# Kernel optimization log

Measured on AMD Instinct MI355X. Metric: run time of the kernel, lower is better.

The kernel has to match this reference:

```python
import jax, jax.numpy as jnp
import numpy as np

N_NODES = 50000
N_EDGES = 800000
HIDDEN = 128
HEADS = 8
HEAD_DIM = HIDDEN // HEADS
N_REL = 64
SCALE = np.sqrt(HEAD_DIM).astype(np.float32)


def setup_inputs() -> dict:
    key = jax.random.key(0)
    ks = jax.random.split(key, 12)
    s = 1.0 / np.sqrt(2 * HIDDEN)
    s2 = 1.0 / np.sqrt(HIDDEN)
    return {
        "node_features": jax.random.normal(ks[0], (N_NODES, HIDDEN), jnp.float32),
        "query_embedding": jax.random.normal(ks[1], (1, HIDDEN), jnp.float32),
        "relation_embeddings": jax.random.normal(ks[2], (N_REL, HIDDEN), jnp.float32),
        "Wq": jax.random.uniform(ks[3], (2 * HIDDEN, HIDDEN), jnp.float32, -s, s),
        "bq": jnp.zeros((HIDDEN,), jnp.float32),
        "Wk": jax.random.uniform(ks[4], (2 * HIDDEN, HIDDEN), jnp.float32, -s, s),
        "bk": jnp.zeros((HIDDEN,), jnp.float32),
        "Wv": jax.random.uniform(ks[5], (HIDDEN, HIDDEN), jnp.float32, -s2, s2),
        "bv": jnp.zeros((HIDDEN,), jnp.float32),
        "Wo": jax.random.uniform(ks[6], (HIDDEN, HIDDEN), jnp.float32, -s2, s2),
        "bo": jnp.zeros((HIDDEN,), jnp.float32),
        "edge_index": jax.random.randint(ks[7], (2, N_EDGES), 0, N_NODES, jnp.int64),
        "edge_type": jax.random.randint(ks[8], (N_EDGES,), 0, N_REL, jnp.int64),
    }


def reference(node_features, query_embedding, relation_embeddings,
              Wq, bq, Wk, bk, Wv, bv, Wo, bo, edge_index, edge_type):
    n = node_features.shape[0]
    # expand query to all nodes and concat: [N, 2*hidden]
    q_exp = jnp.broadcast_to(query_embedding, (n, HIDDEN))
    nq = jnp.concatenate([node_features, q_exp], axis=-1)
    q = (nq @ Wq + bq).reshape(n, HEADS, HEAD_DIM)
    k = (nq @ Wk + bk).reshape(n, HEADS, HEAD_DIM)
    v = (node_features @ Wv + bv).reshape(n, HEADS, HEAD_DIM)

    src, dst = edge_index[0], edge_index[1]
    rel_bias = relation_embeddings[edge_type].reshape(-1, HEADS, HEAD_DIM)

    # edge-wise scores [E, heads]
    scores = jnp.sum(q[dst] * (k[src] + rel_bias), axis=-1) / SCALE

    # sparse softmax grouped by dst; torch init of max buffer is 0 -> clamp at 0
    seg_max = jax.ops.segment_max(scores, dst, num_segments=n)
    seg_max = jnp.maximum(seg_max, 0.0)
    exp_s = jnp.exp(scores - seg_max[dst])
    seg_sum = jax.ops.segment_sum(exp_s, dst, num_segments=n)
    attn = exp_s / (seg_sum[dst] + 1e-8)  # [E, heads]

    messages = attn[:, :, None] * v[src]  # [E, heads, head_dim]
    out = jax.ops.segment_sum(messages, dst, num_segments=n)  # [N, heads, head_dim]
    out = out.reshape(n, HIDDEN)
    return out @ Wo + bo
```

## Files before the change

kernel.cpp:

```cpp
#include <hip/hip_runtime.h>
#include <math.h>

#define N_NODES 50000
#define N_EDGES 800000
#define HID 128
#define HEADS 8
#define HDIM 16
#define CAP 96
#define CNT_BLOCKS 3125
#define QKV_BLOCKS 782

typedef __attribute__((ext_vector_type(8))) short short8;
typedef __attribute__((ext_vector_type(4))) float floatx4;

#if defined(__has_builtin)
#if __has_builtin(__builtin_amdgcn_fdot2_f32_bf16)
#define HAVE_DOT2 1
#endif
#endif
#ifndef HAVE_DOT2
#define HAVE_DOT2 0
#endif

#if HAVE_DOT2
typedef __attribute__((ext_vector_type(2))) __bf16 bf16x2;
__device__ __forceinline__ float dot2acc(unsigned int a, unsigned int b, float c) {
    return __builtin_amdgcn_fdot2_f32_bf16(__builtin_bit_cast(bf16x2, a),
                                           __builtin_bit_cast(bf16x2, b), c, false);
}
#endif

__device__ __forceinline__ float bf_lo(unsigned int d) { return __uint_as_float(d << 16); }
__device__ __forceinline__ float bf_hi(unsigned int d) { return __uint_as_float(d & 0xFFFF0000u); }
__device__ __forceinline__ unsigned short f2bf(float f) {
    unsigned int u = __float_as_uint(f);
    u = (u + 0x7FFFu + ((u >> 16) & 1u)) >> 16;
    return (unsigned short)u;
}
__device__ __forceinline__ unsigned int pack_bf2(float a, float b) {
    return (unsigned int)f2bf(a) | ((unsigned int)f2bf(b) << 16);
}

__global__ __launch_bounds__(256) void prep_kernel(
    const float* __restrict__ query, const float* __restrict__ rel,
    const float* __restrict__ Wq, const float* __restrict__ bq,
    const float* __restrict__ Wk, const float* __restrict__ bk,
    const float* __restrict__ Wv, const float* __restrict__ Wo,
    unsigned short* __restrict__ Wt, unsigned short* __restrict__ relbf,
    int* __restrict__ counts, float* __restrict__ bqe, float* __restrict__ bke) {
    __shared__ float fred[256];
    int b = blockIdx.x, tid = threadIdx.x;
    if (b >= 256) {
        const float* W  = (b == 256) ? Wq : Wk;
        const float* bb = (b == 256) ? bq : bk;
        float* dst      = (b == 256) ? bqe : bke;
        int j = tid & 127;
        int half = tid >> 7;
        float a = 0.0f;
        int i0 = half * 64;
        for (int i = 0; i < 64; ++i) a += query[i0 + i] * W[(HID + i0 + i) * HID + j];
        fred[tid] = a;
        __syncthreads();
        if (half == 0) dst[j] = fred[j] + fred[128 + j] + bb[j];
        return;
    }
    int idx = b * 256 + tid;
    if (idx < N_NODES) counts[idx] = 0;
    if (idx < 64 * HID) relbf[idx] = f2bf(rel[idx]);
    int m = idx >> 14;
    int rem = idx & 16383;
    int n = rem >> 7, k = rem & 127;
    const float* W = (m == 0) ? Wq : (m == 1) ? Wk : (m == 2) ? Wv : Wo;
    Wt[idx] = f2bf(W[k * HID + n]);
}

__global__ __launch_bounds__(256) void qkv_bucket_kernel(
    const float* __restrict__ nf, const unsigned short* __restrict__ Wt,
    const float* __restrict__ bqe, const float* __restrict__ bke, const float* __restrict__ bv,
    const int* __restrict__ ei, const int* __restrict__ et,
    int* __restrict__ counts, unsigned int* __restrict__ slots,
    unsigned short* __restrict__ qb16, unsigned short* __restrict__ kv16) {
    if (blockIdx.x >= QKV_BLOCKS) {
        int e = (blockIdx.x - QKV_BLOCKS) * 256 + threadIdx.x;
        if (e < N_EDGES) {
            int dst = ei[N_EDGES + e];
            int pos = atomicAdd(&counts[dst], 1);
            if (pos < CAP)
                slots[(unsigned)dst * CAP + pos] =
                    ((unsigned int)et[e] << 18) | (unsigned int)ei[e];
        }
        return;
    }
    int row0 = blockIdx.x * 64;
    int wave = threadIdx.x >> 6;
    int lane = threadIdx.x & 63;
    int col  = lane & 15;
    int quad = lane >> 4;

    short8 afr[4][4];
    #pragma unroll
    for (int t = 0; t < 4; ++t) {
        int arow = row0 + t * 16 + col;
        int asafe = (arow < N_NODES) ? arow : (N_NODES - 1);
        #pragma unroll
        for (int kk = 0; kk < 4; ++kk) {
            const float4* ap = (const float4*)(nf + (size_t)asafe * HID + kk * 32 + quad * 8);
            float4 a0 = ap[0], a1 = ap[1];
            short8 f;
            f[0] = (short)f2bf(a0.x); f[1] = (short)f2bf(a0.y);
            f[2] = (short)f2bf(a0.z); f[3] = (short)f2bf(a0.w);
            f[4] = (short)f2bf(a1.x); f[5] = (short)f2bf(a1.y);
            f[6] = (short)f2bf(a1.z); f[7] = (short)f2bf(a1.w);
            afr[t][kk] = f;
        }
    }
    const float* biases[3] = {bqe, bke, bv};
    #pragma unroll
    for (int m = 0; m < 3; ++m) {
        const unsigned short* W = Wt + (size_t)m * HID * HID;
        #pragma unroll
        for (int nn = 0; nn < 2; ++nn) {
            int n = wave * 2 + nn;
            float b = biases[m][n * 16 + col];
            floatx4 acc[4];
            #pragma unroll
            for (int t = 0; t < 4; ++t) acc[t] = (floatx4){b, b, b, b};
            short8 bfr[4];
            #pragma unroll
            for (int kk = 0; kk < 4; ++kk)
                bfr[kk] = *(const short8*)(W + (size_t)(n * 16 + col) * HID + kk * 32 + quad * 8);
            #pragma unroll
            for (int kk = 0; kk < 4; ++kk)
                #pragma unroll
                for (int t = 0; t < 4; ++t)
                    acc[t] = __builtin_amdgcn_mfma_f32_16x16x32_bf16(afr[t][kk], bfr[kk], acc[t], 0, 0, 0);
            #pragma unroll
            for (int t = 0; t < 4; ++t) {
                #pragma unroll
                for (int i = 0; i < 4; ++i) {
                    int r = row0 + t * 16 + quad * 4 + i;
                    if (r < N_NODES) {
                        int c = n * 16 + col;
                        if (m == 0)      qb16[(size_t)r * HID + c] = f2bf(acc[t][i]);
                        else if (m == 1) kv16[(size_t)r * 256 + c] = f2bf(acc[t][i]);
                        else             kv16[(size_t)r * 256 + 128 + c] = f2bf(acc[t][i]);
                    }
                }
            }
        }
    }
}

__global__ __launch_bounds__(256) void attn_kernel(
    const unsigned int* __restrict__ qb, const unsigned int* __restrict__ kvu,
    const unsigned int* __restrict__ relu,
    const int* __restrict__ counts, const unsigned int* __restrict__ slots,
    unsigned int* __restrict__ abuf) {
    int node = blockIdx.x * 4 + (threadIdx.x >> 6);
    int lane = threadIdx.x & 63;
    int h = lane & 7;
    int hd = lane >> 3;
    int deg = counts[node];
    if (deg > CAP) deg = CAP;
    unsigned int rs = (unsigned)node * CAP;

    const uint4* qp = (const uint4*)(qb + (unsigned)node * 64 + h * 8);
    uint4 qa = qp[0], qc = qp[1];
#if !HAVE_DOT2
    float qf0 = bf_lo(qa.x), qf1 = bf_hi(qa.x), qf2 = bf_lo(qa.y), qf3 = bf_hi(qa.y);
    float qf4 = bf_lo(qa.z), qf5 = bf_hi(qa.z), qf6 = bf_lo(qa.w), qf7 = bf_hi(qa.w);
    float qf8 = bf_lo(qc.x), qf9 = bf_hi(qc.x), qf10 = bf_lo(qc.y), qf11 = bf_hi(qc.y);
    float qf12 = bf_lo(qc.z), qf13 = bf_hi(qc.z), qf14 = bf_lo(qc.w), qf15 = bf_hi(qc.w);
#endif

    int myel = hd;
    unsigned int pk = (myel < deg) ? slots[rs + myel] : 0u;
    float ssum = 0.0f, accx = 0.0f, accy = 0.0f;
    for (int base = 0; base < deg; base += 8) {
        int el = base + myel;
        int eln = el + 8;
        unsigned int pk_next = (eln < deg) ? slots[rs + eln] : 0u;
        unsigned int pw = 0u;
        if (el < deg) {
            unsigned int src = pk & 0x3FFFF;
            unsigned int etv = pk >> 18;
            const uint4* kp = (const uint4*)(kvu + (src << 7) + h * 8);
            uint4 ka = kp[0], kb = kp[1];
            const uint4* rp = (const uint4*)(relu + (etv << 6) + h * 8);
            uint4 ra = rp[0], rb = rp[1];
            float s;
#if HAVE_DOT2
            float s0 = dot2acc(qa.x, ka.x, 0.0f);
            float s1 = dot2acc(qa.y, ka.y, 0.0f);
            float s2 = dot2acc(qa.z, ka.z, 0.0f);
            float s3 = dot2acc(qa.w, ka.w, 0.0f);
            s0 = dot2acc(qc.x, kb.x, s0);
            s1 = dot2acc(qc.y, kb.y, s1);
            s2 = dot2acc(qc.z, kb.z, s2);
            s3 = dot2acc(qc.w, kb.w, s3);
            s0 = dot2acc(qa.x, ra.x, s0);
            s1 = dot2acc(qa.y, ra.y, s1);
            s2 = dot2acc(qa.z, ra.z, s2);
            s3 = dot2acc(qa.w, ra.w, s3);
            s0 = dot2acc(qc.x, rb.x, s0);
            s1 = dot2acc(qc.y, rb.y, s1);
            s2 = dot2acc(qc.z, rb.z, s2);
            s3 = dot2acc(qc.w, rb.w, s3);
            s = (s0 + s1) + (s2 + s3);
#else
            float s0 = qf0 * (bf_lo(ka.x) + bf_lo(ra.x)) + qf4 * (bf_lo(ka.z) + bf_lo(ra.z))
                     + qf8 * (bf_lo(kb.x) + bf_lo(rb.x)) + qf12 * (bf_lo(kb.z) + bf_lo(rb.z));
            float s1 = qf1 * (bf_hi(ka.x) + bf_hi(ra.x)) + qf5 * (bf_hi(ka.z) + bf_hi(ra.z))
                     + qf9 * (bf_hi(kb.x) + bf_hi(rb.x)) + qf13 * (bf_hi(kb.z) + bf_hi(rb.z));
            float s2 = qf2 * (bf_lo(ka.y) + bf_lo(ra.y)) + qf6 * (bf_lo(ka.w) + bf_lo(ra.w))
                     + qf10 * (bf_lo(kb.y) + bf_lo(rb.y)) + qf14 * (bf_lo(kb.w) + bf_lo(rb.w));
            float s3 = qf3 * (bf_hi(ka.y) + bf_hi(ra.y)) + qf7 * (bf_hi(ka.w) + bf_hi(ra.w))
                     + qf11 * (bf_hi(kb.y) + bf_hi(rb.y)) + qf15 * (bf_hi(kb.w) + bf_hi(rb.w));
            s = (s0 + s1) + (s2 + s3);
#endif
            float w = __expf(s * 0.25f);
            unsigned int wb = (unsigned int)f2bf(w);
            ssum += __uint_as_float(wb << 16);
            pw = (wb << 16) | src;
        }
        #pragma unroll
        for (int j = 0; j < 8; ++j) {
            unsigned int pj = __shfl(pw, j * 8 + hd);
            float wj = bf_hi(pj);
            unsigned int sj = pj & 0xFFFFu;
            unsigned int vp = kvu[(sj << 7) + 64 + lane];
            accx += wj * bf_lo(vp);
            accy += wj * bf_hi(vp);
        }
        pk = pk_next;
    }
    #pragma unroll
    for (int off = 8; off < 64; off <<= 1) ssum += __shfl_xor(ssum, off);
    float inv = 1.0f / (__shfl(ssum, hd) + 1e-8f);
    abuf[(unsigned)node * 64 + lane] = pack_bf2(accx * inv, accy * inv);
}

__global__ __launch_bounds__(256) void out_mfma_kernel(
    const unsigned short* __restrict__ abuf, const unsigned short* __restrict__ Wot,
    const float* __restrict__ bo, float* __restrict__ out) {
    int row0 = blockIdx.x * 64;
    int wave = threadIdx.x >> 6;
    int lane = threadIdx.x & 63;
    int col  = lane & 15;
    int quad = lane >> 4;

    short8 afr[4][4];
    #pragma unroll
    for (int t = 0; t < 4; ++t) {
        int arow = row0 + t * 16 + col;
        int asafe = (arow < N_NODES) ? arow : (N_NODES - 1);
        #pragma unroll
        for (int kk = 0; kk < 4; ++kk)
            afr[t][kk] = *(const short8*)(abuf + (size_t)asafe * HID + kk * 32 + quad * 8);
    }

    #pragma unroll
    for (int nn = 0; nn < 2; ++nn) {
        int n = wave * 2 + nn;
        float b = bo[n * 16 + col];
        floatx4 acc[4];
        #pragma unroll
        for (int t = 0; t < 4; ++t) acc[t] = (floatx4){b, b, b, b};
        short8 bfr[4];
        #pragma unroll
        for (int kk = 0; kk < 4; ++kk)
            bfr[kk] = *(const short8*)(Wot + (size_t)(n * 16 + col) * HID + kk * 32 + quad * 8);
        #pragma unroll
        for (int kk = 0; kk < 4; ++kk)
            #pragma unroll
            for (int t = 0; t < 4; ++t)
                acc[t] = __builtin_amdgcn_mfma_f32_16x16x32_bf16(afr[t][kk], bfr[kk], acc[t], 0, 0, 0);
        #pragma unroll
        for (int t = 0; t < 4; ++t) {
            #pragma unroll
            for (int i = 0; i < 4; ++i) {
                int r = row0 + t * 16 + quad * 4 + i;
                if (r < N_NODES) out[(size_t)r * HID + n * 16 + col] = acc[t][i];
            }
        }
    }
}

extern "C" void kernel_launch(void* const* d_in, const int* in_sizes, int n_in,
                              void* d_out, int out_size, void* d_ws, size_t ws_size,
                              hipStream_t stream) {
    const float* nf    = (const float*)d_in[0];
    const float* query = (const float*)d_in[1];
    const float* rel   = (const float*)d_in[2];
    const float* Wq    = (const float*)d_in[3];
    const float* bq    = (const float*)d_in[4];
    const float* Wk    = (const float*)d_in[5];
    const float* bk    = (const float*)d_in[6];
    const float* Wv    = (const float*)d_in[7];
    const float* bv    = (const float*)d_in[8];
    const float* Wo    = (const float*)d_in[9];
    const float* bo    = (const float*)d_in[10];
    const int*   ei    = (const int*)d_in[11];
    const int*   et    = (const int*)d_in[12];
    float* out = (float*)d_out;

    char* ws = (char*)d_ws;
    unsigned short* qb16 = (unsigned short*)ws; ws += (size_t)N_NODES * HID * 2;
    unsigned short* kv16 = (unsigned short*)ws; ws += (size_t)N_NODES * 256 * 2;
    unsigned int* abuf   = (unsigned int*)ws;   ws += (size_t)N_NODES * 64 * 4;
    float* bqe           = (float*)ws;          ws += 128 * 4;
    float* bke           = (float*)ws;          ws += 128 * 4;
    int* counts          = (int*)ws;            ws += (size_t)N_NODES * 4;
    unsigned int* slots  = (unsigned int*)ws;   ws += (size_t)N_NODES * CAP * 4;
    unsigned short* Wt   = (unsigned short*)ws; ws += (size_t)4 * HID * HID * 2;
    unsigned short* relbf = (unsigned short*)ws; ws += (size_t)64 * HID * 2;

    prep_kernel<<<258, 256, 0, stream>>>(query, rel, Wq, bq, Wk, bk, Wv, Wo,
                                         Wt, relbf, counts, bqe, bke);
    qkv_bucket_kernel<<<QKV_BLOCKS + CNT_BLOCKS, 256, 0, stream>>>(
        nf, Wt, bqe, bke, bv, ei, et, counts, slots, qb16, kv16);
    attn_kernel<<<N_NODES / 4, 256, 0, stream>>>(
        (const unsigned int*)qb16, (const unsigned int*)kv16,
        (const unsigned int*)relbf, counts, slots, abuf);
    out_mfma_kernel<<<QKV_BLOCKS, 256, 0, stream>>>(
        (const unsigned short*)abuf, Wt + (size_t)3 * HID * HID, bo, out);
}
```

Before: 236.6 us.

## Pre-convert node features to bf16 and split bucketing from QKV kernel

Result: slower. 251.0 us (+6.1%).

```diff
diff --git a/kernel.cpp b/kernel.cpp
--- a/kernel.cpp
+++ b/kernel.cpp
@@ -9,6 +9,7 @@
 #define CAP 96
 #define CNT_BLOCKS 3125
 #define QKV_BLOCKS 782
+#define NFB_BLOCKS 3125
 
 typedef __attribute__((ext_vector_type(8))) short short8;
 typedef __attribute__((ext_vector_type(4))) float floatx4;
@@ -42,14 +43,28 @@
 }
 
 __global__ __launch_bounds__(256) void prep_kernel(
+    const float* __restrict__ nf,
     const float* __restrict__ query, const float* __restrict__ rel,
     const float* __restrict__ Wq, const float* __restrict__ bq,
     const float* __restrict__ Wk, const float* __restrict__ bk,
     const float* __restrict__ Wv, const float* __restrict__ Wo,
     unsigned short* __restrict__ Wt, unsigned short* __restrict__ relbf,
-    int* __restrict__ counts, float* __restrict__ bqe, float* __restrict__ bke) {
+    int* __restrict__ counts, float* __restrict__ bqe, float* __restrict__ bke,
+    unsigned short* __restrict__ nfb) {
     __shared__ float fred[256];
     int b = blockIdx.x, tid = threadIdx.x;
+    if (b >= 258) {
+        int base = (b - 258) * 2048 + tid * 8;
+        const float4* p = (const float4*)(nf + base);
+        float4 a0 = p[0], a1 = p[1];
+        short8 f;
+        f[0] = (short)f2bf(a0.x); f[1] = (short)f2bf(a0.y);
+        f[2] = (short)f2bf(a0.z); f[3] = (short)f2bf(a0.w);
+        f[4] = (short)f2bf(a1.x); f[5] = (short)f2bf(a1.y);
+        f[6] = (short)f2bf(a1.z); f[7] = (short)f2bf(a1.w);
+        *(short8*)(nfb + base) = f;
+        return;
+    }
     if (b >= 256) {
         const float* W  = (b == 256) ? Wq : Wk;
         const float* bb = (b == 256) ? bq : bk;
@@ -74,23 +89,23 @@
     Wt[idx] = f2bf(W[k * HID + n]);
 }
 
-__global__ __launch_bounds__(256) void qkv_bucket_kernel(
-    const float* __restrict__ nf, const unsigned short* __restrict__ Wt,
+__global__ __launch_bounds__(256) void bucket_kernel(
+    const int* __restrict__ ei, const int* __restrict__ et,
+    int* __restrict__ counts, unsigned int* __restrict__ slots) {
+    int e = blockIdx.x * 256 + threadIdx.x;
+    if (e < N_EDGES) {
+        int dst = ei[N_EDGES + e];
+        int pos = atomicAdd(&counts[dst], 1);
+        if (pos < CAP)
+            slots[(unsigned)dst * CAP + pos] =
+                ((unsigned int)et[e] << 18) | (unsigned int)ei[e];
+    }
+}
+
+__global__ __launch_bounds__(256) void qkv_kernel(
+    const unsigned short* __restrict__ nfb, const unsigned short* __restrict__ Wt,
     const float* __restrict__ bqe, const float* __restrict__ bke, const float* __restrict__ bv,
-    const int* __restrict__ ei, const int* __restrict__ et,
-    int* __restrict__ counts, unsigned int* __restrict__ slots,
     unsigned short* __restrict__ qb16, unsigned short* __restrict__ kv16) {
-    if (blockIdx.x >= QKV_BLOCKS) {
-        int e = (blockIdx.x - QKV_BLOCKS) * 256 + threadIdx.x;
-        if (e < N_EDGES) {
-            int dst = ei[N_EDGES + e];
-            int pos = atomicAdd(&counts[dst], 1);
-            if (pos < CAP)
-                slots[(unsigned)dst * CAP + pos] =
-                    ((unsigned int)et[e] << 18) | (unsigned int)ei[e];
-        }
-        return;
-    }
     int row0 = blockIdx.x * 64;
     int wave = threadIdx.x >> 6;
     int lane = threadIdx.x & 63;
@@ -103,16 +118,8 @@
         int arow = row0 + t * 16 + col;
         int asafe = (arow < N_NODES) ? arow : (N_NODES - 1);
         #pragma unroll
-        for (int kk = 0; kk < 4; ++kk) {
-            const float4* ap = (const float4*)(nf + (size_t)asafe * HID + kk * 32 + quad * 8);
-            float4 a0 = ap[0], a1 = ap[1];
-            short8 f;
-            f[0] = (short)f2bf(a0.x); f[1] = (short)f2bf(a0.y);
-            f[2] = (short)f2bf(a0.z); f[3] = (short)f2bf(a0.w);
-            f[4] = (short)f2bf(a1.x); f[5] = (short)f2bf(a1.y);
-            f[6] = (short)f2bf(a1.z); f[7] = (short)f2bf(a1.w);
-            afr[t][kk] = f;
-        }
+        for (int kk = 0; kk < 4; ++kk)
+            afr[t][kk] = *(const short8*)(nfb + (size_t)asafe * HID + kk * 32 + quad * 8);
     }
     const float* biases[3] = {bqe, bke, bv};
     #pragma unroll
@@ -314,11 +321,12 @@
     unsigned int* slots  = (unsigned int*)ws;   ws += (size_t)N_NODES * CAP * 4;
     unsigned short* Wt   = (unsigned short*)ws; ws += (size_t)4 * HID * HID * 2;
     unsigned short* relbf = (unsigned short*)ws; ws += (size_t)64 * HID * 2;
-
-    prep_kernel<<<258, 256, 0, stream>>>(query, rel, Wq, bq, Wk, bk, Wv, Wo,
-                                         Wt, relbf, counts, bqe, bke);
-    qkv_bucket_kernel<<<QKV_BLOCKS + CNT_BLOCKS, 256, 0, stream>>>(
-        nf, Wt, bqe, bke, bv, ei, et, counts, slots, qb16, kv16);
+    unsigned short* nfb  = (unsigned short*)ws; ws += (size_t)N_NODES * HID * 2;
+
+    prep_kernel<<<258 + NFB_BLOCKS, 256, 0, stream>>>(nf, query, rel, Wq, bq, Wk, bk, Wv, Wo,
+                                                      Wt, relbf, counts, bqe, bke, nfb);
+    bucket_kernel<<<CNT_BLOCKS, 256, 0, stream>>>(ei, et, counts, slots);
+    qkv_kernel<<<QKV_BLOCKS, 256, 0, stream>>>(nfb, Wt, bqe, bke, bv, qb16, kv16);
     attn_kernel<<<N_NODES / 4, 256, 0, stream>>>(
         (const unsigned int*)qb16, (const unsigned int*)kv16,
         (const unsigned int*)relbf, counts, slots, abuf);
```
